# Performance work log

Hardware: AMD Instinct MI355X
Metric: run time of the kernel (lower is better)

The kernel has to match this reference:

```python
import jax, jax.numpy as jnp
import numpy as np

NEG_INF = -9.0e15

def setup_inputs() -> dict:
    key = jax.random.key(0)
    k1, k2, k3, k4, k5 = jax.random.split(key, 5)
    B, N, I, H, D = 4, 2048, 256, 4, 64  # batch, nodes, input_dim, heads, head_dim
    E = H * D
    X = jax.random.normal(k1, (B, N, I), dtype=jnp.float32)
    A = jax.random.randint(k2, (B, N, N), 0, 2, dtype=jnp.int32)
    # xavier_uniform with gain 1.38675
    g = 1.38675
    lim_W = g * np.sqrt(6.0 / (I + D))
    W = jax.random.uniform(k3, (H, I, D), minval=-lim_W, maxval=lim_W, dtype=jnp.float32)
    lim_a = g * np.sqrt(6.0 / (2 * D + 1))
    a = jax.random.uniform(k4, (H, 2 * D, 1), minval=-lim_a, maxval=lim_a, dtype=jnp.float32)
    lim_o = np.sqrt(1.0 / E)
    W_out = jax.random.uniform(k5, (E, E), minval=-lim_o, maxval=lim_o, dtype=jnp.float32)
    b_out = jnp.zeros((E,), dtype=jnp.float32)
    return {"X": X, "A": A, "W": W, "a": a, "W_out": W_out, "b_out": b_out}

def reference(X, A, W, a, W_out, b_out):
    B, N, _ = X.shape
    H_heads, _, D = W.shape
    # per-head projection: [b, h, n, d]
    Hp = jnp.einsum('bni,hid->bhnd', X, W)
    # additive attention scores (src/dst halves of a)
    H1 = jnp.einsum('bhnd,hd->bhn', Hp, a[:, :D, 0])   # [b,h,n]
    H2 = jnp.einsum('bhnd,hd->bhn', Hp, a[:, D:, 0])   # [b,h,n]
    E = jax.nn.leaky_relu(H1[:, :, :, None] + H2[:, :, None, :], negative_slope=0.2)  # [b,h,N,N]
    att = jnp.where(A[:, None, :, :] > 0, E, NEG_INF)
    # NOTE: faithful to original torch code: softmax over dim=1 (heads axis)
    att = jax.nn.softmax(att, axis=1)
    Hprime = jnp.einsum('bhNn,bhnd->bhNd', att, Hp)  # [b,h,N,d]
    # faithful raw reshape (no transpose), matching torch .reshape semantics
    Hprime = Hprime.reshape(B, N, H_heads * D)
    out = Hprime @ W_out.T + b_out
    return out
```

## Files before the change

### kernel.cpp

```cpp
#include <hip/hip_runtime.h>

constexpr int B = 4, N = 2048, I = 256, H = 4, D = 64, E = 256;
constexpr float LOG2E = 1.44269504088896340736f;

typedef __bf16 bf16x8 __attribute__((ext_vector_type(8)));
typedef float f32x4 __attribute__((ext_vector_type(4)));
typedef unsigned short us8 __attribute__((ext_vector_type(8)));

#if __has_builtin(__builtin_amdgcn_exp2f)
#define EXP2(x) __builtin_amdgcn_exp2f(x)
#else
#define EXP2(x) __expf((x) * 0.69314718055994530942f)
#endif

__device__ __forceinline__ unsigned short f2bf(float f) {
    unsigned u = __builtin_bit_cast(unsigned, f);
    u = (u + 0x7FFFu + ((u >> 16) & 1u)) >> 16;
    return (unsigned short)u;
}
__device__ __forceinline__ float bf2f(unsigned short s) {
    return __builtin_bit_cast(float, (unsigned)s << 16);
}

constexpr int CH = 4096;
constexpr int PROJ_BLKS = 256;
constexpr int PACK_BLKS = B * N / 4;

__global__ __launch_bounds__(256) void k_wconv(const float* __restrict__ Wo,
                                               const float* __restrict__ W,
                                               unsigned short* __restrict__ WoF,
                                               unsigned short* __restrict__ WfF) {
    int bid = blockIdx.x;
    int t = threadIdx.x;
    if (bid < 32) {
        int gid = bid * 256 + t;
        int l = gid & 63, ks = (gid >> 6) & 7, et = gid >> 9;
        int row = et * 16 + (l & 15);
        int col = ks * 32 + (l >> 4) * 8;
        const float* src = Wo + (size_t)row * E + col;
        us8 hi, lo;
        #pragma unroll
        for (int e = 0; e < 8; ++e) {
            float v = src[e];
            unsigned short hb = f2bf(v);
            hi[e] = hb;
            lo[e] = f2bf(v - bf2f(hb));
        }
        ((us8*)WoF)[gid] = hi;
        ((us8*)WoF)[8192 + gid] = lo;
    } else {
        int gid = (bid - 32) * 256 + t;
        int l = gid & 63, ks = (gid >> 6) & 7, et = gid >> 9;
        int c = et * 16 + (l & 15);
        int h = c >> 6, d = c & 63;
        int k0 = ks * 32 + (l >> 4) * 8;
        const float* src = W + ((size_t)h * I + k0) * D + d;
        us8 hi, lo;
        #pragma unroll
        for (int e = 0; e < 8; ++e) {
            float v = src[(size_t)e * D];
            unsigned short hb = f2bf(v);
            hi[e] = hb;
            lo[e] = f2bf(v - bf2f(hb));
        }
        ((us8*)WfF)[gid] = hi;
        ((us8*)WfF)[8192 + gid] = lo;
    }
}

__global__ __launch_bounds__(256) void k_prep(const float* __restrict__ X,
                                              const int* __restrict__ A,
                                              const float* __restrict__ a,
                                              const unsigned short* __restrict__ WfF,
                                              unsigned short* __restrict__ HpF,
                                              float* __restrict__ H1,
                                              float* __restrict__ H2i,
                                              unsigned int* __restrict__ Abits) {
    __shared__ float ldsT[4][16 * 132];

    int bid = blockIdx.x;
    int t = threadIdx.x;

    if (bid < PROJ_BLKS) {
        int wv = t >> 6, l = t & 63;
        int u = bid * 4 + wv;
        int eh = u & 1;
        int rt = u >> 1;
        int b = rt >> 7;
        int n0 = (rt & 127) * 16;
        int m = l & 15;
        int kh = l >> 4;

        const float* Xrow = X + ((size_t)b * N + n0 + m) * I + kh * 8;
        const us8* wf = (const us8*)WfF;

        f32x4 acc[8] = {};

        #pragma unroll
        for (int ks = 0; ks < 8; ++ks) {
            float4 xa = *(const float4*)(Xrow + ks * 32);
            float4 xb = *(const float4*)(Xrow + ks * 32 + 4);
            float xv[8] = {xa.x, xa.y, xa.z, xa.w, xb.x, xb.y, xb.z, xb.w};
            bf16x8 xh, xl;
            #pragma unroll
            for (int e = 0; e < 8; ++e) {
                unsigned short hb = f2bf(xv[e]);
                xh[e] = __builtin_bit_cast(__bf16, hb);
                xl[e] = __builtin_bit_cast(__bf16, f2bf(xv[e] - bf2f(hb)));
            }
            #pragma unroll
            for (int etl = 0; etl < 8; ++etl) {
                int et = eh * 8 + etl;
                bf16x8 wh = __builtin_bit_cast(bf16x8, wf[(size_t)(et * 8 + ks) * 64 + l]);
                bf16x8 wl = __builtin_bit_cast(bf16x8, wf[8192 + (size_t)(et * 8 + ks) * 64 + l]);
                acc[etl] = __builtin_amdgcn_mfma_f32_16x16x32_bf16(xh, wh, acc[etl], 0, 0, 0);
                acc[etl] = __builtin_amdgcn_mfma_f32_16x16x32_bf16(xl, wh, acc[etl], 0, 0, 0);
                acc[etl] = __builtin_amdgcn_mfma_f32_16x16x32_bf16(xh, wl, acc[etl], 0, 0, 0);
            }
        }

        float a1v[8], a2v[8];
        #pragma unroll
        for (int etl = 0; etl < 8; ++etl) {
            int c = eh * 128 + etl * 16 + m;
            int h = c >> 6, d = c & 63;
            a1v[etl] = a[h * (2 * D) + d];
            a2v[etl] = a[h * (2 * D) + D + d];
        }
        #pragma unroll
        for (int hh = 0; hh < 2; ++hh) {
            #pragma unroll
            for (int r = 0; r < 4; ++r) {
                float s1 = 0.f, s2 = 0.f;
                #pragma unroll
                for (int q = 0; q < 4; ++q) {
                    s1 += acc[hh * 4 + q][r] * a1v[hh * 4 + q];
                    s2 += acc[hh * 4 + q][r] * a2v[hh * 4 + q];
                }
                #pragma unroll
                for (int off = 1; off < 16; off <<= 1) {
                    s1 += __shfl_xor(s1, off, 64);
                    s2 += __shfl_xor(s2, off, 64);
                }
                if (m == 0) {
                    int hg = eh * 2 + hh;
                    int row = kh * 4 + r;
                    H1[(size_t)(b * H + hg) * N + n0 + row] = s1 * LOG2E;
                    H2i[((size_t)b * N + n0 + row) * H + hg] = s2 * LOG2E;
                }
            }
        }

        float* lw = ldsT[wv];
        #pragma unroll
        for (int etl = 0; etl < 8; ++etl)
            #pragma unroll
            for (int r = 0; r < 4; ++r)
                lw[(kh * 4 + r) * 132 + etl * 16 + m] = acc[etl][r];

        #pragma unroll
        for (int cc = 0; cc < 4; ++cc) {
            int ci = cc * 64 + l;
            int c_local = ci >> 1, q = ci & 1;
            us8 o;
            #pragma unroll
            for (int e = 0; e < 8; ++e)
                o[e] = f2bf(lw[(q * 8 + e) * 132 + c_local]);
            int cg = eh * 128 + c_local;
            int h = cg >> 6, d = cg & 63;
            int nb = n0 + q * 8;
            int jblk = nb >> 5, g = (nb >> 3) & 3;
            ((us8*)HpF)[(((size_t)(b * H + h) * 64 + jblk) * 4 + (d >> 4)) * 64 + ((d & 15) + 16 * g)] = o;
        }

    } else {
        int blk = bid - PROJ_BLKS;
        int w = blk * 4 + (t >> 6);
        int l = t & 63;
        int b = w >> 11;
        int i = w & 2047;
        const int4* Arow = (const int4*)(A + (size_t)w * N);
        unsigned int* dstb = Abits + (size_t)b * 64 * 2048 + i;
        #pragma unroll
        for (int c = 0; c < 8; ++c) {
            int4 v = Arow[c * 64 + l];
            unsigned nib = ((unsigned)v.x | ((unsigned)v.y << 1) |
                            ((unsigned)v.z << 2) | ((unsigned)v.w << 3)) << ((l & 7) * 4);
            nib |= __shfl_xor((int)nib, 1, 64);
            nib |= __shfl_xor((int)nib, 2, 64);
            nib |= __shfl_xor((int)nib, 4, 64);
            if ((l & 7) == 0) dstb[(size_t)(c * 8 + (l >> 3)) * 2048] = nib;
        }
    }
}

constexpr int NSTEP = 8;

__global__ __launch_bounds__(256) void k_agg(const unsigned int* __restrict__ Abits,
                                             const float* __restrict__ H1,
                                             const float* __restrict__ H2i,
                                             const unsigned short* __restrict__ HpF,
                                             unsigned short* __restrict__ part) {
    __shared__ unsigned short red[4][CH];

    int bid = blockIdx.x;
    int b  = bid & 3;
    int jh = (bid >> 2) & 1;
    int it = bid >> 3;
    int t = threadIdx.x;
    int wv = t >> 6, l = t & 63;
    int i0 = it * 16;
    int jb = jh * 1024 + wv * 256;
    int jt0 = jb >> 5;
    int row = l & 15;
    int kg  = l >> 4;

    float h1v[H];
    #pragma unroll
    for (int h = 0; h < H; ++h) h1v[h] = H1[(size_t)(b * H + h) * N + i0 + row];

    f32x4 acc[H][4] = {};

    const unsigned int* Abp = Abits + (size_t)b * 64 * 2048 + i0 + row;
    const float4* H2r = (const float4*)(H2i + ((size_t)b * N + jb + kg * 8) * H);
    const us8* Hf = (const us8*)HpF + ((size_t)(b * H) * 64 + jt0) * 256 + l;

    unsigned int aw = Abp[(size_t)jt0 * 2048];

    #pragma unroll 2
    for (int s = 0; s < NSTEP; ++s) {
        int sn = (s + 1 < NSTEP) ? (s + 1) : s;
        unsigned int awn = Abp[(size_t)(jt0 + sn) * 2048];

        bf16x8 af[H];
        #pragma unroll
        for (int e = 0; e < 8; ++e) {
            bool on = (aw >> (kg * 8 + e)) & 1u;
            float4 h2 = H2r[s * 32 + e];
            float v0 = h1v[0] + h2.x;
            float v1 = h1v[1] + h2.y;
            float v2 = h1v[2] + h2.z;
            float v3 = h1v[3] + h2.w;
            float s0 = on ? fmaxf(v0, 0.2f * v0) : 0.f;
            float s1 = on ? fmaxf(v1, 0.2f * v1) : 0.f;
            float s2 = on ? fmaxf(v2, 0.2f * v2) : 0.f;
            float s3 = on ? fmaxf(v3, 0.2f * v3) : 0.f;
            float e0 = EXP2(s0);
            float e1 = EXP2(s1);
            float e2 = EXP2(s2);
            float e3 = EXP2(s3);
            float zi = __builtin_amdgcn_rcpf(e0 + e1 + e2 + e3);
            af[0][e] = (__bf16)(e0 * zi);
            af[1][e] = (__bf16)(e1 * zi);
            af[2][e] = (__bf16)(e2 * zi);
            af[3][e] = (__bf16)(e3 * zi);
        }

        __builtin_amdgcn_s_setprio(1);
        #pragma unroll
        for (int h = 0; h < H; ++h) {
            #pragma unroll
            for (int nt = 0; nt < 4; ++nt) {
                bf16x8 bfr = __builtin_bit_cast(bf16x8, Hf[(size_t)h * 64 * 256 + s * 256 + nt * 64]);
                acc[h][nt] = __builtin_amdgcn_mfma_f32_16x16x32_bf16(af[h], bfr, acc[h][nt], 0, 0, 0);
            }
        }
        __builtin_amdgcn_s_setprio(0);

        aw = awn;
    }

    #pragma unroll
    for (int h = 0; h < H; ++h)
        #pragma unroll
        for (int nt = 0; nt < 4; ++nt)
            #pragma unroll
            for (int r = 0; r < 4; ++r)
                red[wv][(((h * 4 + nt) * 4 + r)) * 64 + l] = f2bf(acc[h][nt][r]);
    __syncthreads();

    unsigned short* chunk = part + (((size_t)jh * B + b) * 128 + it) * CH;
    #pragma unroll
    for (int k = 0; k < CH / 256; ++k) {
        int idx = t + 256 * k;
        float s = bf2f(red[0][idx]) + bf2f(red[1][idx]) + bf2f(red[2][idx]) + bf2f(red[3][idx]);
        chunk[idx] = f2bf(s);
    }
}

__global__ __launch_bounds__(256) void k_out(const unsigned short* __restrict__ part,
                                             const unsigned short* __restrict__ WoF,
                                             const float* __restrict__ bo,
                                             float* __restrict__ out) {
    int bid = blockIdx.x;
    int eh  = bid & 1;
    int itg = (bid >> 1) & 31;
    int b   = bid >> 6;
    int t = threadIdx.x;
    int h = t >> 6, l = t & 63;
    int it0 = itg * 4;
    int m = l & 15;
    int it = it0 + (m >> 2), kg = m & 3;
    int kh = l >> 4;

    const unsigned short* c0 = part + ((size_t)(0 * B + b) * 128 + it) * CH;
    const unsigned short* c1 = part + ((size_t)(1 * B + b) * 128 + it) * CH;
    const us8* wf = (const us8*)WoF;

    f32x4 acc[8] = {};

    #pragma unroll
    for (int ks = 0; ks < 8; ++ks) {
        int k0 = ks * 32 + kh * 8;
        int nt = (k0 >> 4) & 3, r = k0 >> 6, rw0 = k0 & 15;
        int cidx = ((h * 4 + nt) * 4 + r) * 64 + kg * 16 + rw0;
        us8 p0 = *(const us8*)(c0 + cidx);
        us8 p1 = *(const us8*)(c1 + cidx);
        bf16x8 af;
        #pragma unroll
        for (int e = 0; e < 8; ++e) af[e] = (__bf16)(bf2f(p0[e]) + bf2f(p1[e]));

        #pragma unroll
        for (int etl = 0; etl < 8; ++etl) {
            int et = eh * 8 + etl;
            bf16x8 bh = __builtin_bit_cast(bf16x8, wf[(size_t)(et * 8 + ks) * 64 + l]);
            bf16x8 bl = __builtin_bit_cast(bf16x8, wf[8192 + (size_t)(et * 8 + ks) * 64 + l]);
            acc[etl] = __builtin_amdgcn_mfma_f32_16x16x32_bf16(af, bh, acc[etl], 0, 0, 0);
            acc[etl] = __builtin_amdgcn_mfma_f32_16x16x32_bf16(af, bl, acc[etl], 0, 0, 0);
        }
    }

    #pragma unroll
    for (int etl = 0; etl < 8; ++etl) {
        int e = (eh * 8 + etl) * 16 + (l & 15);
        float bias = bo[e];
        #pragma unroll
        for (int rr = 0; rr < 4; ++rr) {
            int nprime = h * 512 + (it0 + (l >> 4)) * 4 + rr;
            out[((size_t)b * N + nprime) * E + e] = acc[etl][rr] + bias;
        }
    }
}

extern "C" void kernel_launch(void* const* d_in, const int* in_sizes, int n_in,
                              void* d_out, int out_size, void* d_ws, size_t ws_size,
                              hipStream_t stream) {
    const float* X  = (const float*)d_in[0];
    const int*   A  = (const int*)d_in[1];
    const float* W  = (const float*)d_in[2];
    const float* a  = (const float*)d_in[3];
    const float* Wo = (const float*)d_in[4];
    const float* bo = (const float*)d_in[5];
    float* out = (float*)d_out;

    unsigned short* wsu  = (unsigned short*)d_ws;
    unsigned short* part = wsu;
    unsigned short* HpF  = wsu + (size_t)2 * B * 128 * CH;
    float* H1  = (float*)(HpF + (size_t)B * H * D * N);
    float* H2i = H1 + B * H * N;
    unsigned int* Abits = (unsigned int*)(H2i + (size_t)B * N * H);
    unsigned short* WoF = (unsigned short*)(Abits + (size_t)B * 64 * 2048);
    unsigned short* WfF = WoF + 2 * 8192 * 8;

    k_wconv<<<dim3(64), dim3(256), 0, stream>>>(Wo, W, WoF, WfF);
    k_prep<<<dim3(PROJ_BLKS + PACK_BLKS), dim3(256), 0, stream>>>(
        X, A, a, WfF, HpF, H1, H2i, Abits);
    k_agg<<<dim3(2 * B * 128), dim3(256), 0, stream>>>(Abits, H1, H2i, HpF, part);
    k_out<<<dim3(B * 32 * 2), dim3(256), 0, stream>>>(part, WoF, bo, out);
}
```

Baseline: 105.8 us.

## Fuse output projection into aggregation kernel with 8-wave blocks covering full j range

The aggregation kernel now uses 512 threads so one block covers all 2048 source nodes. This removes the two-way j split and the global partial buffer. The eight wave partials are reduced in shared memory, and the W_out projection plus bias is applied in the same kernel, which drops the separate k_out launch and its round trip through global memory. In exchange, the block count is halved, shared memory per block doubles to 64KB, and the output GEMM uses only a small share of the MFMA work per block, which may cut occupancy.

```diff
diff --git a/kernel.cpp b/kernel.cpp
--- a/kernel.cpp
+++ b/kernel.cpp
@@ -196,22 +196,23 @@
 
 constexpr int NSTEP = 8;
 
-__global__ __launch_bounds__(256) void k_agg(const unsigned int* __restrict__ Abits,
+__global__ __launch_bounds__(512) void k_agg(const unsigned int* __restrict__ Abits,
                                              const float* __restrict__ H1,
                                              const float* __restrict__ H2i,
                                              const unsigned short* __restrict__ HpF,
-                                             unsigned short* __restrict__ part) {
-    __shared__ unsigned short red[4][CH];
+                                             const unsigned short* __restrict__ WoF,
+                                             const float* __restrict__ bo,
+                                             float* __restrict__ out) {
+    __shared__ unsigned short red[8][CH];
 
     int bid = blockIdx.x;
     int b  = bid & 3;
-    int jh = (bid >> 2) & 1;
-    int it = bid >> 3;
+    int it = bid >> 2;
     int t = threadIdx.x;
     int wv = t >> 6, l = t & 63;
     int i0 = it * 16;
-    int jb = jh * 1024 + wv * 256;
-    int jt0 = jb >> 5;
+    int jb = wv * 256;
+    int jt0 = wv * 8;
     int row = l & 15;
     int kg  = l >> 4;
 
@@ -279,65 +280,53 @@
                 red[wv][(((h * 4 + nt) * 4 + r)) * 64 + l] = f2bf(acc[h][nt][r]);
     __syncthreads();
 
-    unsigned short* chunk = part + (((size_t)jh * B + b) * 128 + it) * CH;
-    #pragma unroll
-    for (int k = 0; k < CH / 256; ++k) {
-        int idx = t + 256 * k;
-        float s = bf2f(red[0][idx]) + bf2f(red[1][idx]) + bf2f(red[2][idx]) + bf2f(red[3][idx]);
-        chunk[idx] = f2bf(s);
-    }
-}
-
-__global__ __launch_bounds__(256) void k_out(const unsigned short* __restrict__ part,
-                                             const unsigned short* __restrict__ WoF,
-                                             const float* __restrict__ bo,
-                                             float* __restrict__ out) {
-    int bid = blockIdx.x;
-    int eh  = bid & 1;
-    int itg = (bid >> 1) & 31;
-    int b   = bid >> 6;
-    int t = threadIdx.x;
-    int h = t >> 6, l = t & 63;
-    int it0 = itg * 4;
-    int m = l & 15;
-    int it = it0 + (m >> 2), kg = m & 3;
-    int kh = l >> 4;
-
-    const unsigned short* c0 = part + ((size_t)(0 * B + b) * 128 + it) * CH;
-    const unsigned short* c1 = part + ((size_t)(1 * B + b) * 128 + it) * CH;
+    {
+        int idx8 = t * 8;
+        float s8[8] = {0.f, 0.f, 0.f, 0.f, 0.f, 0.f, 0.f, 0.f};
+        #pragma unroll
+        for (int slot = 0; slot < 8; ++slot) {
+            us8 raw = *(const us8*)&red[slot][idx8];
+            #pragma unroll
+            for (int e = 0; e < 8; ++e) s8[e] += bf2f(raw[e]);
+        }
+        us8 o;
+        #pragma unroll
+        for (int e = 0; e < 8; ++e) o[e] = f2bf(s8[e]);
+        *(us8*)&red[0][idx8] = o;
+    }
+    __syncthreads();
+
     const us8* wf = (const us8*)WoF;
-
-    f32x4 acc[8] = {};
+    f32x4 acc2[2] = {};
 
     #pragma unroll
     for (int ks = 0; ks < 8; ++ks) {
-        int k0 = ks * 32 + kh * 8;
-        int nt = (k0 >> 4) & 3, r = k0 >> 6, rw0 = k0 & 15;
-        int cidx = ((h * 4 + nt) * 4 + r) * 64 + kg * 16 + rw0;
-        us8 p0 = *(const us8*)(c0 + cidx);
-        us8 p1 = *(const us8*)(c1 + cidx);
-        bf16x8 af;
-        #pragma unroll
-        for (int e = 0; e < 8; ++e) af[e] = (__bf16)(bf2f(p0[e]) + bf2f(p1[e]));
-
-        #pragma unroll
-        for (int etl = 0; etl < 8; ++etl) {
-            int et = eh * 8 + etl;
+        int kk = ks * 32 + (l >> 4) * 8;
+        int c = kk >> 6, d0 = kk & 63;
+        int nt2 = d0 >> 4, dl = d0 & 15;
+        int h2 = (l & 15) >> 2, g = (l & 15) & 3;
+        int ridx = (((h2 * 4 + nt2) * 4 + c) * 64 + g * 16 + dl);
+        bf16x8 afr = *(const bf16x8*)&red[0][ridx];
+
+        #pragma unroll
+        for (int etl = 0; etl < 2; ++etl) {
+            int et = wv * 2 + etl;
             bf16x8 bh = __builtin_bit_cast(bf16x8, wf[(size_t)(et * 8 + ks) * 64 + l]);
             bf16x8 bl = __builtin_bit_cast(bf16x8, wf[8192 + (size_t)(et * 8 + ks) * 64 + l]);
-            acc[etl] = __builtin_amdgcn_mfma_f32_16x16x32_bf16(af, bh, acc[etl], 0, 0, 0);
-            acc[etl] = __builtin_amdgcn_mfma_f32_16x16x32_bf16(af, bl, acc[etl], 0, 0, 0);
+            acc2[etl] = __builtin_amdgcn_mfma_f32_16x16x32_bf16(afr, bh, acc2[etl], 0, 0, 0);
+            acc2[etl] = __builtin_amdgcn_mfma_f32_16x16x32_bf16(afr, bl, acc2[etl], 0, 0, 0);
         }
     }
 
     #pragma unroll
-    for (int etl = 0; etl < 8; ++etl) {
-        int e = (eh * 8 + etl) * 16 + (l & 15);
+    for (int etl = 0; etl < 2; ++etl) {
+        int e = (wv * 2 + etl) * 16 + (l & 15);
         float bias = bo[e];
         #pragma unroll
         for (int rr = 0; rr < 4; ++rr) {
-            int nprime = h * 512 + (it0 + (l >> 4)) * 4 + rr;
-            out[((size_t)b * N + nprime) * E + e] = acc[etl][rr] + bias;
+            int mprime = (l >> 4) * 4 + rr;
+            int nprime = (mprime >> 2) * 512 + it * 4 + (mprime & 3);
+            out[((size_t)b * N + nprime) * E + e] = acc2[etl][rr] + bias;
         }
     }
 }
@@ -353,9 +342,8 @@
     const float* bo = (const float*)d_in[5];
     float* out = (float*)d_out;
 
-    unsigned short* wsu  = (unsigned short*)d_ws;
-    unsigned short* part = wsu;
-    unsigned short* HpF  = wsu + (size_t)2 * B * 128 * CH;
+    unsigned short* wsu = (unsigned short*)d_ws;
+    unsigned short* HpF = wsu;
     float* H1  = (float*)(HpF + (size_t)B * H * D * N);
     float* H2i = H1 + B * H * N;
     unsigned int* Abits = (unsigned int*)(H2i + (size_t)B * N * H);
@@ -365,6 +353,5 @@
     k_wconv<<<dim3(64), dim3(256), 0, stream>>>(Wo, W, WoF, WfF);
     k_prep<<<dim3(PROJ_BLKS + PACK_BLKS), dim3(256), 0, stream>>>(
         X, A, a, WfF, HpF, H1, H2i, Abits);
-    k_agg<<<dim3(2 * B * 128), dim3(256), 0, stream>>>(Abits, H1, H2i, HpF, part);
-    k_out<<<dim3(B * 32 * 2), dim3(256), 0, stream>>>(part, WoF, bo, out);
-}
+    k_agg<<<dim3(B * 128), dim3(512), 0, stream>>>(Abits, H1, H2i, HpF, WoF, bo, out);
+}
```

New measurement: 91.50 us, median of 2. 13.5% less time.
